# Kernel tuning notes

Measured on AMD Instinct MI355X. Metric: run time of the kernel, lower is better.

Reference implementation:

```python
import jax, jax.numpy as jnp
import numpy as np

B, NSV, NTRK, K, H = 512, 128, 512, 8, 16


def setup_inputs() -> dict:
    key = jax.random.key(0)
    ks = jax.random.split(key, 12)
    p = lambda k, shp: (jax.random.normal(k, shp, dtype=jnp.float32) * 0.1)
    return {
        "x_sv": jax.random.normal(ks[0], (B * NSV, 2), dtype=jnp.float32),
        "x_trk": jax.random.normal(ks[1], (B * NTRK, 8), dtype=jnp.float32),
        "batch_sv": jnp.repeat(jnp.arange(B, dtype=jnp.int32), NSV),
        "batch_trk": jnp.repeat(jnp.arange(B, dtype=jnp.int32), NTRK),
        # sv_encode: Linear(2,16) -> ELU -> Linear(16,16)
        "W1s": p(ks[2], (2, H)), "b1s": jnp.zeros((H,), jnp.float32),
        "W2s": p(ks[3], (H, H)), "b2s": jnp.zeros((H,), jnp.float32),
        # trk_encode: Linear(8,16) -> ELU -> Linear(16,16)
        "W1t": p(ks[4], (8, H)), "b1t": jnp.zeros((H,), jnp.float32),
        "W2t": p(ks[5], (H, H)), "b2t": jnp.zeros((H,), jnp.float32),
        # edge MLP: Linear(2*16, 16)
        "We": p(ks[6], (2 * H, H)), "be": jnp.zeros((H,), jnp.float32),
        # output head: Linear(16, 1)
        "Wo": p(ks[7], (H, 1)), "bo": jnp.zeros((1,), jnp.float32),
    }


def reference(x_sv, x_trk, batch_sv, batch_trk,
              W1s, b1s, W2s, b2s, W1t, b1t, W2t, b2t, We, be, Wo, bo):
    # Node encoders
    sv = jax.nn.elu(x_sv @ W1s + b1s) @ W2s + b2s      # [Nsv, H]
    trk = jax.nn.elu(x_trk @ W1t + b1t) @ W2t + b2t    # [Ntrk, H]

    # Regular batching: reshape to per-event blocks (batch_sv/batch_trk are
    # contiguous repeats of arange(B) with NSV / NTRK nodes per event).
    svb = sv.reshape(B, NSV, H)      # [B, S, H]
    trkb = trk.reshape(B, NTRK, H)   # [B, T, H]

    # kNN in encoded space: squared L2 distance per event, k nearest SVs per track
    t_sq = jnp.sum(trkb * trkb, -1)[:, :, None]          # [B, T, 1]
    s_sq = jnp.sum(svb * svb, -1)[:, None, :]            # [B, 1, S]
    dots = jnp.einsum("bth,bsh->bts", trkb, svb)         # [B, T, S]
    d2 = t_sq + s_sq - 2.0 * dots                        # [B, T, S]
    _, idx = jax.lax.top_k(-d2, K)                       # [B, T, K] indices into S

    # Gather neighbor SV features: [B, T, K, H]
    nbr = jax.vmap(lambda s, i: s[i])(svb, idx)

    # EdgeConv message: nn(cat[x_i, x_j - x_i]), x_i = track (target), x_j = SV
    ti = trkb[:, :, None, :]                                    # [B, T, 1, H]
    msg_in = jnp.concatenate(
        [jnp.broadcast_to(ti, nbr.shape), nbr - ti], axis=-1)   # [B, T, K, 2H]
    msg = msg_in @ We + be                                      # [B, T, K, H]
    feats = jnp.max(msg, axis=2).reshape(B * NTRK, H)           # max aggregation

    # Output head + per-event average pool (avg_pool_x with cluster == batch)
    out = jax.nn.sigmoid(feats @ Wo + bo)                       # [Ntrk, 1]
    sums = jax.ops.segment_sum(out, batch_trk, num_segments=B)  # [B, 1]
    cnts = jax.ops.segment_sum(jnp.ones_like(out), batch_trk, num_segments=B)
    pooled = sums / cnts                                        # [B, 1]
    batch_out = jnp.arange(B, dtype=jnp.int32)
    return pooled, batch_out
```

## Files before the change

### kernel.cpp

```cpp
#include <hip/hip_runtime.h>
#include <cmath>

#define BB   512
#define NSV  128
#define NTRK 512
#define KK   8
#define HH   16
#define TPB  512
#define RSTR 20
#define PSTR 20

typedef float vf2 __attribute__((ext_vector_type(2)));

__device__ __forceinline__ float elu_f(float x) {
    return x > 0.0f ? x : expm1f(x);
}
__device__ __forceinline__ unsigned umin_u(unsigned a, unsigned b) { return a < b ? a : b; }
__device__ __forceinline__ unsigned med3u(unsigned a, unsigned b, unsigned c) {
    unsigned d;
    asm("v_med3_u32 %0, %1, %2, %3" : "=v"(d) : "v"(a), "v"(b), "v"(c));
    return d;
}

__global__ __launch_bounds__(TPB, 4) void fused_all(
    const float* __restrict__ x_sv, const float* __restrict__ x_trk,
    const float* __restrict__ W1s, const float* __restrict__ b1s,
    const float* __restrict__ W2s, const float* __restrict__ b2s,
    const float* __restrict__ W1t, const float* __restrict__ b1t,
    const float* __restrict__ W2t, const float* __restrict__ b2t,
    const float* __restrict__ We,  const float* __restrict__ be,
    const float* __restrict__ Wo,  const float* __restrict__ bo,
    float* __restrict__ svw,
    const float* __restrict__ svr,
    float* __restrict__ out)
{
    __shared__ float proj[NSV][PSTR];
    __shared__ float ucS[HH + 1];
    __shared__ float sred[TPB / 64];

    const int b = blockIdx.x, tid = threadIdx.x;

    if (tid < NSV) {
        const float* xp = x_sv + (size_t)(b * NSV + tid) * 2;
        float x0 = xp[0], x1 = xp[1];
        float hb[HH];
        #pragma unroll
        for (int h = 0; h < HH; ++h)
            hb[h] = elu_f(x0 * W1s[h] + x1 * W1s[HH + h] + b1s[h]);
        float o[HH], sq = 0.0f;
        #pragma unroll
        for (int h2 = 0; h2 < HH; ++h2) {
            float a = b2s[h2];
            #pragma unroll
            for (int h = 0; h < HH; ++h) a += hb[h] * W2s[h * HH + h2];
            o[h2] = a;
            sq += a * a;
        }
        float* dst = svw + (size_t)(b * NSV + tid) * RSTR;
        #pragma unroll
        for (int h4 = 0; h4 < 4; ++h4)
            *(float4*)&dst[h4 * 4] = make_float4(o[h4*4], o[h4*4+1], o[h4*4+2], o[h4*4+3]);
        dst[HH] = 0.5f * sq;
        #pragma unroll
        for (int h = 0; h < HH; ++h) {
            float a = 0.0f;
            #pragma unroll
            for (int j = 0; j < HH; ++j) a += o[j] * We[(HH + j) * HH + h];
            proj[tid][h] = a;
        }
    } else if (tid < NSV + HH) {
        int j = tid - NSV;
        float a = 0.0f;
        #pragma unroll
        for (int h = 0; h < HH; ++h)
            a += (We[j * HH + h] - We[(HH + j) * HH + h]) * Wo[h];
        ucS[j] = a;
    } else if (tid == NSV + HH) {
        float a = bo[0];
        #pragma unroll
        for (int h = 0; h < HH; ++h) a += be[h] * Wo[h];
        ucS[HH] = a;
    }

    float tf[HH], htsq;
    vf2 ntfp[8];
    {
        const float* xp = x_trk + (size_t)(b * NTRK + tid) * 8;
        float x[8];
        *(float4*)&x[0] = *(const float4*)&xp[0];
        *(float4*)&x[4] = *(const float4*)&xp[4];
        float hb[HH];
        #pragma unroll
        for (int h = 0; h < HH; ++h) {
            float a = b1t[h];
            #pragma unroll
            for (int i = 0; i < 8; ++i) a += x[i] * W1t[i * HH + h];
            hb[h] = elu_f(a);
        }
        float sq = 0.0f;
        #pragma unroll
        for (int h2 = 0; h2 < HH; ++h2) {
            float a = b2t[h2];
            #pragma unroll
            for (int h = 0; h < HH; ++h) a += hb[h] * W2t[h * HH + h2];
            tf[h2] = a;
            sq += a * a;
        }
        htsq = 0.5f * sq;
        #pragma unroll
        for (int j = 0; j < 8; ++j) {
            vf2 t; t.x = -tf[2 * j]; t.y = -tf[2 * j + 1];
            ntfp[j] = t;
        }
    }

    unsigned k[KK];
    #pragma unroll
    for (int q = 0; q < KK; ++q) k[q] = 0xFFFFFFFFu;

    __syncthreads();

    const float* rp = svr + (size_t)b * NSV * RSTR;

    vf2 pa[8], pb[8]; float ha, hbv;

    #define LOADROW(buf, hv, idx)                                      \
        do {                                                           \
            const float* _r = rp + (size_t)(idx) * RSTR;               \
            _Pragma("unroll")                                          \
            for (int _j = 0; _j < 8; ++_j)                             \
                buf[_j] = *(const vf2*)(_r + 2 * _j);                  \
            hv = _r[HH];                                               \
        } while (0)

    #define BODY(buf, hv, idx)                                         \
        do {                                                           \
            vf2 a0 = ntfp[0] * buf[0];                                 \
            vf2 a1 = ntfp[1] * buf[1];                                 \
            vf2 a2 = ntfp[2] * buf[2];                                 \
            vf2 a3 = ntfp[3] * buf[3];                                 \
            a0 = __builtin_elementwise_fma(ntfp[4], buf[4], a0);       \
            a1 = __builtin_elementwise_fma(ntfp[5], buf[5], a1);       \
            a2 = __builtin_elementwise_fma(ntfp[6], buf[6], a2);       \
            a3 = __builtin_elementwise_fma(ntfp[7], buf[7], a3);       \
            a0 = a0 + a1; a2 = a2 + a3; a0 = a0 + a2;                  \
            float e = fmaxf((htsq + hv) + (a0.x + a0.y), 0.0f);        \
            unsigned v = (__float_as_uint(e) & 0xFFFFFF80u)            \
                         | (unsigned)(idx);                            \
            unsigned nk0 = umin_u(v, k[0]);                            \
            unsigned nk1 = med3u(v, k[0], k[1]);                       \
            unsigned nk2 = med3u(v, k[1], k[2]);                       \
            unsigned nk3 = med3u(v, k[2], k[3]);                       \
            unsigned nk4 = med3u(v, k[3], k[4]);                       \
            unsigned nk5 = med3u(v, k[4], k[5]);                       \
            unsigned nk6 = med3u(v, k[5], k[6]);                       \
            unsigned nk7 = med3u(v, k[6], k[7]);                       \
            k[0] = nk0; k[1] = nk1; k[2] = nk2; k[3] = nk3;            \
            k[4] = nk4; k[5] = nk5; k[6] = nk6; k[7] = nk7;            \
        } while (0)

    LOADROW(pa, ha, 0);
    LOADROW(pb, hbv, 1);
    for (int s = 0; s < NSV - 2; s += 2) {
        BODY(pa, ha, s);
        LOADROW(pa, ha, s + 2);
        BODY(pb, hbv, s + 1);
        LOADROW(pb, hbv, s + 3);
    }
    BODY(pa, ha, NSV - 2);
    BODY(pb, hbv, NSV - 1);

    #undef LOADROW
    #undef BODY

    float local;
    {
        float acc = ucS[HH];
        #pragma unroll
        for (int j = 0; j < HH; ++j) acc = fmaf(tf[j], ucS[j], acc);

        float mx[HH];
        #pragma unroll
        for (int h = 0; h < HH; ++h) mx[h] = -INFINITY;
        #pragma unroll
        for (int q = 0; q < KK; ++q) {
            const float* pr = &proj[k[q] & 127u][0];
            #pragma unroll
            for (int h4 = 0; h4 < 4; ++h4) {
                float4 p = *(const float4*)&pr[h4 * 4];
                mx[h4 * 4 + 0] = fmaxf(mx[h4 * 4 + 0], p.x);
                mx[h4 * 4 + 1] = fmaxf(mx[h4 * 4 + 1], p.y);
                mx[h4 * 4 + 2] = fmaxf(mx[h4 * 4 + 2], p.z);
                mx[h4 * 4 + 3] = fmaxf(mx[h4 * 4 + 3], p.w);
            }
        }
        #pragma unroll
        for (int h = 0; h < HH; ++h) acc = fmaf(mx[h], Wo[h], acc);
        local = 1.0f / (1.0f + expf(-acc));
    }

    #pragma unroll
    for (int off = 32; off > 0; off >>= 1)
        local += __shfl_down(local, off, 64);
    if ((tid & 63) == 0) sred[tid >> 6] = local;
    __syncthreads();
    if (tid == 0) {
        float tot = 0.0f;
        #pragma unroll
        for (int w = 0; w < TPB / 64; ++w) tot += sred[w];
        out[b]      = tot * (1.0f / NTRK);
        out[BB + b] = (float)b;
    }
}

extern "C" void kernel_launch(void* const* d_in, const int* in_sizes, int n_in,
                              void* d_out, int out_size, void* d_ws, size_t ws_size,
                              hipStream_t stream) {
    const float* x_sv  = (const float*)d_in[0];
    const float* x_trk = (const float*)d_in[1];
    const float* W1s = (const float*)d_in[4];
    const float* b1s = (const float*)d_in[5];
    const float* W2s = (const float*)d_in[6];
    const float* b2s = (const float*)d_in[7];
    const float* W1t = (const float*)d_in[8];
    const float* b1t = (const float*)d_in[9];
    const float* W2t = (const float*)d_in[10];
    const float* b2t = (const float*)d_in[11];
    const float* We  = (const float*)d_in[12];
    const float* be  = (const float*)d_in[13];
    const float* Wo  = (const float*)d_in[14];
    const float* bo  = (const float*)d_in[15];
    float* out = (float*)d_out;

    float* rows = (float*)d_ws;

    fused_all<<<BB, TPB, 0, stream>>>(x_sv, x_trk,
                                      W1s, b1s, W2s, b2s,
                                      W1t, b1t, W2t, b2t,
                                      We, be, Wo, bo,
                                      rows, rows, out);
}
```

Before: 125.3 us.

## Keep SV rows in LDS and broadcast them via readlane in the kNN scan

The encoded SV rows no longer go through a global workspace. They are written to shared memory, then each wave loads two rows per lane into registers and broadcasts them to all lanes with v_readlane (scalar operands) while scanning. This removes the global round-trip and the per-iteration vector loads of the row data. In exchange the inner loop does 17 readlane ops per SV, the packed vf2 FMAs become scalar FMAs, and register pressure rises.

```diff
diff --git a/kernel.cpp b/kernel.cpp
--- a/kernel.cpp
+++ b/kernel.cpp
@@ -10,8 +10,6 @@
 #define RSTR 20
 #define PSTR 20
 
-typedef float vf2 __attribute__((ext_vector_type(2)));
-
 __device__ __forceinline__ float elu_f(float x) {
     return x > 0.0f ? x : expm1f(x);
 }
@@ -21,6 +19,7 @@
     asm("v_med3_u32 %0, %1, %2, %3" : "=v"(d) : "v"(a), "v"(b), "v"(c));
     return d;
 }
+#define RL(x, l) __uint_as_float((unsigned)__builtin_amdgcn_readlane((int)__float_as_uint(x), (l)))
 
 __global__ __launch_bounds__(TPB, 4) void fused_all(
     const float* __restrict__ x_sv, const float* __restrict__ x_trk,
@@ -30,10 +29,9 @@
     const float* __restrict__ W2t, const float* __restrict__ b2t,
     const float* __restrict__ We,  const float* __restrict__ be,
     const float* __restrict__ Wo,  const float* __restrict__ bo,
-    float* __restrict__ svw,
-    const float* __restrict__ svr,
     float* __restrict__ out)
 {
+    __shared__ float rowS[NSV][RSTR];
     __shared__ float proj[NSV][PSTR];
     __shared__ float ucS[HH + 1];
     __shared__ float sred[TPB / 64];
@@ -56,11 +54,9 @@
             o[h2] = a;
             sq += a * a;
         }
-        float* dst = svw + (size_t)(b * NSV + tid) * RSTR;
-        #pragma unroll
-        for (int h4 = 0; h4 < 4; ++h4)
-            *(float4*)&dst[h4 * 4] = make_float4(o[h4*4], o[h4*4+1], o[h4*4+2], o[h4*4+3]);
-        dst[HH] = 0.5f * sq;
+        #pragma unroll
+        for (int h = 0; h < HH; ++h) rowS[tid][h] = o[h];
+        rowS[tid][HH] = 0.5f * sq;
         #pragma unroll
         for (int h = 0; h < HH; ++h) {
             float a = 0.0f;
@@ -83,7 +79,6 @@
     }
 
     float tf[HH], htsq;
-    vf2 ntfp[8];
     {
         const float* xp = x_trk + (size_t)(b * NTRK + tid) * 8;
         float x[8];
@@ -107,11 +102,6 @@
             sq += a * a;
         }
         htsq = 0.5f * sq;
-        #pragma unroll
-        for (int j = 0; j < 8; ++j) {
-            vf2 t; t.x = -tf[2 * j]; t.y = -tf[2 * j + 1];
-            ntfp[j] = t;
-        }
     }
 
     unsigned k[KK];
@@ -120,58 +110,53 @@
 
     __syncthreads();
 
-    const float* rp = svr + (size_t)b * NSV * RSTR;
-
-    vf2 pa[8], pb[8]; float ha, hbv;
-
-    #define LOADROW(buf, hv, idx)                                      \
-        do {                                                           \
-            const float* _r = rp + (size_t)(idx) * RSTR;               \
-            _Pragma("unroll")                                          \
-            for (int _j = 0; _j < 8; ++_j)                             \
-                buf[_j] = *(const vf2*)(_r + 2 * _j);                  \
-            hv = _r[HH];                                               \
-        } while (0)
-
-    #define BODY(buf, hv, idx)                                         \
-        do {                                                           \
-            vf2 a0 = ntfp[0] * buf[0];                                 \
-            vf2 a1 = ntfp[1] * buf[1];                                 \
-            vf2 a2 = ntfp[2] * buf[2];                                 \
-            vf2 a3 = ntfp[3] * buf[3];                                 \
-            a0 = __builtin_elementwise_fma(ntfp[4], buf[4], a0);       \
-            a1 = __builtin_elementwise_fma(ntfp[5], buf[5], a1);       \
-            a2 = __builtin_elementwise_fma(ntfp[6], buf[6], a2);       \
-            a3 = __builtin_elementwise_fma(ntfp[7], buf[7], a3);       \
-            a0 = a0 + a1; a2 = a2 + a3; a0 = a0 + a2;                  \
-            float e = fmaxf((htsq + hv) + (a0.x + a0.y), 0.0f);        \
-            unsigned v = (__float_as_uint(e) & 0xFFFFFF80u)            \
-                         | (unsigned)(idx);                            \
-            unsigned nk0 = umin_u(v, k[0]);                            \
-            unsigned nk1 = med3u(v, k[0], k[1]);                       \
-            unsigned nk2 = med3u(v, k[1], k[2]);                       \
-            unsigned nk3 = med3u(v, k[2], k[3]);                       \
-            unsigned nk4 = med3u(v, k[3], k[4]);                       \
-            unsigned nk5 = med3u(v, k[4], k[5]);                       \
-            unsigned nk6 = med3u(v, k[5], k[6]);                       \
-            unsigned nk7 = med3u(v, k[6], k[7]);                       \
-            k[0] = nk0; k[1] = nk1; k[2] = nk2; k[3] = nk3;            \
-            k[4] = nk4; k[5] = nk5; k[6] = nk6; k[7] = nk7;            \
-        } while (0)
-
-    LOADROW(pa, ha, 0);
-    LOADROW(pb, hbv, 1);
-    for (int s = 0; s < NSV - 2; s += 2) {
-        BODY(pa, ha, s);
-        LOADROW(pa, ha, s + 2);
-        BODY(pb, hbv, s + 1);
-        LOADROW(pb, hbv, s + 3);
-    }
-    BODY(pa, ha, NSV - 2);
-    BODY(pb, hbv, NSV - 1);
-
-    #undef LOADROW
-    #undef BODY
+    const int lane = tid & 63;
+    float rA[17], rB[17];
+    #pragma unroll
+    for (int j4 = 0; j4 < 4; ++j4) {
+        float4 a4 = *(const float4*)&rowS[lane][j4 * 4];
+        float4 b4 = *(const float4*)&rowS[lane + 64][j4 * 4];
+        rA[j4*4+0] = a4.x; rA[j4*4+1] = a4.y; rA[j4*4+2] = a4.z; rA[j4*4+3] = a4.w;
+        rB[j4*4+0] = b4.x; rB[j4*4+1] = b4.y; rB[j4*4+2] = b4.z; rB[j4*4+3] = b4.w;
+    }
+    rA[16] = rowS[lane][HH];
+    rB[16] = rowS[lane + 64][HH];
+
+    #define SCAN(R, base)                                                   \
+        _Pragma("unroll 8")                                                 \
+        for (int s = 0; s < 64; ++s) {                                      \
+            float u[17];                                                    \
+            _Pragma("unroll")                                               \
+            for (int j = 0; j < 17; ++j) u[j] = RL(R[j], s);                \
+            float a0 = -tf[0] * u[0];                                       \
+            float a1 = -tf[1] * u[1];                                       \
+            float a2 = -tf[2] * u[2];                                       \
+            float a3 = -tf[3] * u[3];                                       \
+            _Pragma("unroll")                                               \
+            for (int j = 4; j < 16; j += 4) {                               \
+                a0 = fmaf(-tf[j],     u[j],     a0);                        \
+                a1 = fmaf(-tf[j + 1], u[j + 1], a1);                        \
+                a2 = fmaf(-tf[j + 2], u[j + 2], a2);                        \
+                a3 = fmaf(-tf[j + 3], u[j + 3], a3);                        \
+            }                                                               \
+            float e = fmaxf(((htsq + u[16]) + (a0 + a1)) + (a2 + a3), 0.0f);\
+            unsigned v = (__float_as_uint(e) & 0xFFFFFF80u)                 \
+                         | (unsigned)((base) + s);                          \
+            unsigned nk0 = umin_u(v, k[0]);                                 \
+            unsigned nk1 = med3u(v, k[0], k[1]);                            \
+            unsigned nk2 = med3u(v, k[1], k[2]);                            \
+            unsigned nk3 = med3u(v, k[2], k[3]);                            \
+            unsigned nk4 = med3u(v, k[3], k[4]);                            \
+            unsigned nk5 = med3u(v, k[4], k[5]);                            \
+            unsigned nk6 = med3u(v, k[5], k[6]);                            \
+            unsigned nk7 = med3u(v, k[6], k[7]);                            \
+            k[0] = nk0; k[1] = nk1; k[2] = nk2; k[3] = nk3;                 \
+            k[4] = nk4; k[5] = nk5; k[6] = nk6; k[7] = nk7;                 \
+        }
+
+    SCAN(rA, 0)
+    SCAN(rB, 64)
+    #undef SCAN
 
     float local;
     {
@@ -232,11 +217,8 @@
     const float* bo  = (const float*)d_in[15];
     float* out = (float*)d_out;
 
-    float* rows = (float*)d_ws;
-
     fused_all<<<BB, TPB, 0, stream>>>(x_sv, x_trk,
                                       W1s, b1s, W2s, b2s,
                                       W1t, b1t, W2t, b2t,
-                                      We, be, Wo, bo,
-                                      rows, rows, out);
-}
+                                      We, be, Wo, bo, out);
+}
```

Result: slower. 151.3 us (+20.7%).

## Split SV scan across two thread halves and merge top-k via bitonic min

Applied to the files above, without the earlier changes.

Doubles the block to 1024 threads so each track is processed by two threads, each scanning half of the 128 SVs and keeping its own sorted top-8. The two partial lists are exchanged through a new shared buffer and merged with an elementwise min against the reversed partner list (a bitonic-style merge). Both threads then compute the output, and the pool divides by twice the track count. This halves the serial distance loop per thread at the cost of duplicated encoder and head work, more shared memory, an extra barrier, and possibly lower occupancy.

```diff
diff --git a/kernel.cpp b/kernel.cpp
--- a/kernel.cpp
+++ b/kernel.cpp
@@ -6,9 +6,10 @@
 #define NTRK 512
 #define KK   8
 #define HH   16
-#define TPB  512
+#define TPB  1024
 #define RSTR 20
 #define PSTR 20
+#define KSTR 17
 
 typedef float vf2 __attribute__((ext_vector_type(2)));
 
@@ -22,7 +23,7 @@
     return d;
 }
 
-__global__ __launch_bounds__(TPB, 4) void fused_all(
+__global__ __launch_bounds__(TPB, 8) void fused_all(
     const float* __restrict__ x_sv, const float* __restrict__ x_trk,
     const float* __restrict__ W1s, const float* __restrict__ b1s,
     const float* __restrict__ W2s, const float* __restrict__ b2s,
@@ -34,11 +35,14 @@
     const float* __restrict__ svr,
     float* __restrict__ out)
 {
-    __shared__ float proj[NSV][PSTR];
-    __shared__ float ucS[HH + 1];
-    __shared__ float sred[TPB / 64];
-
-    const int b = blockIdx.x, tid = threadIdx.x;
+    __shared__ float    proj[NSV][PSTR];
+    __shared__ unsigned kbuf[NTRK][KSTR];
+    __shared__ float    ucS[HH + 1];
+    __shared__ float    sred[TPB / 64];
+
+    const int b   = blockIdx.x, tid = threadIdx.x;
+    const int tl  = tid & 511;
+    const int sh  = __builtin_amdgcn_readfirstlane(tid >> 9);
 
     if (tid < NSV) {
         const float* xp = x_sv + (size_t)(b * NSV + tid) * 2;
@@ -85,7 +89,7 @@
     float tf[HH], htsq;
     vf2 ntfp[8];
     {
-        const float* xp = x_trk + (size_t)(b * NTRK + tid) * 8;
+        const float* xp = x_trk + (size_t)(b * NTRK + tl) * 8;
         float x[8];
         *(float4*)&x[0] = *(const float4*)&xp[0];
         *(float4*)&x[4] = *(const float4*)&xp[4];
@@ -120,7 +124,8 @@
 
     __syncthreads();
 
-    const float* rp = svr + (size_t)b * NSV * RSTR;
+    const int sbase = sh * 64;
+    const float* rp = svr + (size_t)(b * NSV + sbase) * RSTR;
 
     vf2 pa[8], pb[8]; float ha, hbv;
 
@@ -146,7 +151,7 @@
             a0 = a0 + a1; a2 = a2 + a3; a0 = a0 + a2;                  \
             float e = fmaxf((htsq + hv) + (a0.x + a0.y), 0.0f);        \
             unsigned v = (__float_as_uint(e) & 0xFFFFFF80u)            \
-                         | (unsigned)(idx);                            \
+                         | (unsigned)(sbase + (idx));                  \
             unsigned nk0 = umin_u(v, k[0]);                            \
             unsigned nk1 = med3u(v, k[0], k[1]);                       \
             unsigned nk2 = med3u(v, k[1], k[2]);                       \
@@ -161,17 +166,28 @@
 
     LOADROW(pa, ha, 0);
     LOADROW(pb, hbv, 1);
-    for (int s = 0; s < NSV - 2; s += 2) {
+    for (int s = 0; s < 64 - 2; s += 2) {
         BODY(pa, ha, s);
         LOADROW(pa, ha, s + 2);
         BODY(pb, hbv, s + 1);
         LOADROW(pb, hbv, s + 3);
     }
-    BODY(pa, ha, NSV - 2);
-    BODY(pb, hbv, NSV - 1);
+    BODY(pa, ha, 62);
+    BODY(pb, hbv, 63);
 
     #undef LOADROW
     #undef BODY
+
+    #pragma unroll
+    for (int q = 0; q < KK; ++q) kbuf[tl][sh * 8 + q] = k[q];
+    __syncthreads();
+
+    unsigned m[KK];
+    {
+        const unsigned* pk = &kbuf[tl][(sh ^ 1) * 8];
+        #pragma unroll
+        for (int i = 0; i < KK; ++i) m[i] = umin_u(k[i], pk[7 - i]);
+    }
 
     float local;
     {
@@ -184,7 +200,7 @@
         for (int h = 0; h < HH; ++h) mx[h] = -INFINITY;
         #pragma unroll
         for (int q = 0; q < KK; ++q) {
-            const float* pr = &proj[k[q] & 127u][0];
+            const float* pr = &proj[m[q] & 127u][0];
             #pragma unroll
             for (int h4 = 0; h4 < 4; ++h4) {
                 float4 p = *(const float4*)&pr[h4 * 4];
@@ -208,7 +224,7 @@
         float tot = 0.0f;
         #pragma unroll
         for (int w = 0; w < TPB / 64; ++w) tot += sred[w];
-        out[b]      = tot * (1.0f / NTRK);
+        out[b]      = tot * (1.0f / (2 * NTRK));
         out[BB + b] = (float)b;
     }
 }
```

Result: slower. 131.1 us (+4.6%).
